# Optimization experiments

Hardware: AMD Instinct MI355X
Metric: run time of the kernel (lower is better)

Reference implementation:

```python
import jax, jax.numpy as jnp
import numpy as np

L = 2          # stacked LSTM layers
E = 4          # ensemble size
B, T, D = 256, 256, 512
H, CTX, HID, OUT = 512, 256, 256, 64


def setup_inputs() -> dict:
    key = jax.random.key(0)
    ks = jax.random.split(key, 16)
    w = lambda k, s, sc: (jax.random.normal(k, s, jnp.float32) * sc)
    r1 = lambda k, s: 1.0 + 0.05 * jax.random.normal(k, s, jnp.float32)
    lstm_b = jnp.zeros((L, E, 4 * H), jnp.float32).at[:, :, H:2 * H].set(1.0)  # unit forget bias
    return {
        'sequence_embeddings': jax.random.normal(ks[0], (B, T, D), jnp.float32),
        'context_embeddings': jax.random.normal(ks[1], (B, CTX), jnp.float32),
        'sequence_length': jax.random.randint(ks[2], (B,), 1, T + 1, jnp.int32),
        'lstm_W': w(ks[3], (L, D, 4 * H), 0.02),
        'lstm_U': w(ks[4], (L, H, 4 * H), 0.02),
        'lstm_b': lstm_b,
        'lstm_alpha': r1(ks[5], (L, E, D)),
        'lstm_gamma': r1(ks[6], (L, E, 4 * H)),
        'lstm_ralpha': r1(ks[7], (L, E, H)),
        'lstm_rgamma': r1(ks[8], (L, E, 4 * H)),
        'hid_W': w(ks[9], (H + CTX, HID), 0.05),
        'hid_b': jnp.zeros((E, HID), jnp.float32),
        'hid_alpha': r1(ks[10], (E, H + CTX)),
        'hid_gamma': r1(ks[11], (E, HID)),
        'out_W': w(ks[12], (HID, OUT), 0.05),
        'out_b': jnp.zeros((E, OUT), jnp.float32),
        'out_alpha': r1(ks[13], (E, HID)),
        'out_gamma': r1(ks[14], (E, OUT)),
    }


def reference(sequence_embeddings, context_embeddings, sequence_length,
              lstm_W, lstm_U, lstm_b, lstm_alpha, lstm_gamma, lstm_ralpha, lstm_rgamma,
              hid_W, hid_b, hid_alpha, hid_gamma,
              out_W, out_b, out_alpha, out_gamma):
    Bv, Tv, _ = sequence_embeddings.shape
    Hv = lstm_U.shape[1]
    per = Bv // E  # examples per ensemble member (consecutive blocks)
    exp = lambda p: jnp.repeat(p, per, axis=1)        # [L,E,d] -> [L,B,d]
    aF, gF = exp(lstm_alpha), exp(lstm_gamma)
    raF, rgF = exp(lstm_ralpha), exp(lstm_rgamma)
    bF = exp(lstm_b)

    dt = sequence_embeddings.dtype
    mask = (jnp.arange(Tv)[None, :] < sequence_length[:, None]).astype(dt)  # [B,T]
    xs = (jnp.swapaxes(sequence_embeddings, 0, 1), mask.T[..., None])       # [T,B,D], [T,B,1]

    def step(carry, xm):
        hs, cs = carry
        x, m = xm
        inp = x
        new_h, new_c = [], []
        for l in range(L):
            h, c = hs[l], cs[l]
            # rank-1 multiplicative perturbations fused with gate matmuls
            z = ((inp * aF[l]) @ lstm_W[l]) * gF[l] \
                + ((h * raF[l]) @ lstm_U[l]) * rgF[l] + bF[l]
            i, f, g, o = jnp.split(z, 4, axis=-1)
            c_n = jax.nn.sigmoid(f) * c + jax.nn.sigmoid(i) * jnp.tanh(g)
            h_n = jax.nn.sigmoid(o) * jnp.tanh(c_n)
            h_n = jnp.where(m > 0, h_n, h)  # masked steps carry state through
            c_n = jnp.where(m > 0, c_n, c)
            new_h.append(h_n)
            new_c.append(c_n)
            inp = h_n
        return (jnp.stack(new_h), jnp.stack(new_c)), None

    init = (jnp.zeros((L, Bv, Hv), dt), jnp.zeros((L, Bv, Hv), dt))
    (hs, _), _ = jax.lax.scan(step, init, xs)
    feat = jnp.concatenate([hs[-1], context_embeddings], axis=-1)

    def dense_r1(x, Wt, bt, al, ga, act=None):
        af = jnp.repeat(al, per, axis=0)
        gf = jnp.repeat(ga, per, axis=0)
        bf = jnp.repeat(bt, per, axis=0)
        y = ((x * af) @ Wt) * gf + bf
        return act(y) if act is not None else y

    relu6 = lambda v: jnp.clip(v, 0.0, 6.0)
    hidden = dense_r1(feat, hid_W, hid_b, hid_alpha, hid_gamma, relu6)
    return dense_r1(hidden, out_W, out_b, out_alpha, out_gamma)
```

## Files before the change

### kernel.cpp

```cpp
#include <hip/hip_runtime.h>
#include <cstdint>
#include <cstddef>


typedef __attribute__((ext_vector_type(8))) short  s16x8;
typedef __attribute__((ext_vector_type(8))) __bf16 bf16x8;
typedef __attribute__((ext_vector_type(4))) float  f32x4;
typedef unsigned long long ull;

__device__ __forceinline__ short f2bfs(float f) {
  union { float f; unsigned u; } v; v.f = f;
  unsigned r = v.u + 0x7FFFu + ((v.u >> 16) & 1u);
  return (short)(r >> 16);
}
__device__ __forceinline__ float bf2f(short s) {
  union { unsigned u; float f; } v; v.u = ((unsigned)(unsigned short)s) << 16;
  return v.f;
}
__device__ __forceinline__ void split2(float v, short& hi, short& lo) {
  hi = f2bfs(v);
  lo = f2bfs(v - bf2f(hi));
}
__device__ __forceinline__ float sigf(float x) { return 1.0f / (1.0f + __expf(-x)); }

__device__ __forceinline__ void unpack_pk(const uint4 r0, const uint4 r1,
                                          s16x8& hi, s16x8& lo) {
  uint4 hv, lv;
  hv.x = __builtin_amdgcn_perm(r0.y, r0.x, 0x05040100u);
  lv.x = __builtin_amdgcn_perm(r0.y, r0.x, 0x07060302u);
  hv.y = __builtin_amdgcn_perm(r0.w, r0.z, 0x05040100u);
  lv.y = __builtin_amdgcn_perm(r0.w, r0.z, 0x07060302u);
  hv.z = __builtin_amdgcn_perm(r1.y, r1.x, 0x05040100u);
  lv.z = __builtin_amdgcn_perm(r1.y, r1.x, 0x07060302u);
  hv.w = __builtin_amdgcn_perm(r1.w, r1.z, 0x05040100u);
  lv.w = __builtin_amdgcn_perm(r1.w, r1.z, 0x07060302u);
  hi = __builtin_bit_cast(s16x8, hv);
  lo = __builtin_bit_cast(s16x8, lv);
}

__device__ __forceinline__ void barrier_rb(unsigned* rbBase, int wgLocal,
                                           unsigned tstep) {
  __syncthreads();
  if (threadIdx.x < 64) {
    const int lane = threadIdx.x;
    int rel = 0;
    if (lane == 0) {
      const int c = wgLocal >> 3;
      unsigned a = __hip_atomic_fetch_add(rbBase + c * 16, 1u,
                                          __ATOMIC_RELAXED, __HIP_MEMORY_SCOPE_AGENT);
      if (a == 8u * tstep - 1u) {
        unsigned r = __hip_atomic_fetch_add(rbBase + 128, 1u,
                                            __ATOMIC_RELAXED, __HIP_MEMORY_SCOPE_AGENT);
        if (r == 8u * tstep - 1u) rel = 1;
      }
    }
    rel = __shfl(rel, 0);
    unsigned* flags = rbBase + 256;
    if (rel) {
      __hip_atomic_store(flags + lane * 16, tstep,
                         __ATOMIC_RELAXED, __HIP_MEMORY_SCOPE_AGENT);
    } else if (lane == 0) {
      int spins = 0;
      while (__hip_atomic_load(flags + wgLocal * 16, __ATOMIC_RELAXED,
                               __HIP_MEMORY_SCOPE_AGENT) < tstep) {
        __builtin_amdgcn_s_sleep(1);
        if (++spins > (1 << 22)) break;
      }
    }
    if (lane == 0)
      __builtin_amdgcn_fence(__ATOMIC_ACQUIRE, "agent");
  }
  __syncthreads();
}

#define REDOFF 131072

__global__ __launch_bounds__(512, 1) void lstm_persist(
    const unsigned* __restrict__ seqP,
    unsigned* __restrict__ h0P, unsigned* __restrict__ h1P,
    const short* __restrict__ Wf, const float* __restrict__ biasF,
    const int* __restrict__ slen, unsigned* __restrict__ bar)
{
  extern __shared__ __align__(16) char bsw[];
  const int wg = blockIdx.x;
  const int cls = wg & 7;
  const int layer = cls >> 2;
  const int rb = cls & 3;
  const int cb = wg >> 3;
  const int tid = threadIdx.x;
  const int wave = tid >> 6, lane = tid & 63;
  const int kh = wave >> 2, ws = wave & 3;
  const int wgLocal = (layer << 5) | cb;

  const short* Wfe = Wf + ((size_t)(layer * 4 + rb) * 2048 + cb * 64) * 1024;
  #pragma unroll
  for (int i = 0; i < 16; ++i) {
    int f = (i << 9) + tid;
    int col = f >> 7, fr = f & 127;
    s16x8 v = *reinterpret_cast<const s16x8*>(Wfe + (size_t)col * 1024 + (fr << 3));
    int byo = (fr << 10) + (((col << 4)) ^ ((fr & 7) << 4));
    *reinterpret_cast<s16x8*>(bsw + byo) = v;
  }
  __syncthreads();

  const int j = lane & 15;
  const int g = lane >> 4;
  const int koff = g << 3;
  const int rowg = rb * 64 + ws * 16 + j;
  const int rbase = rb * 64 + ws * 16 + (g << 2);
  const int u = cb * 16 + j;
  const float* bp = biasF + (size_t)(layer * 4 + rb) * 2048 + cb * 64 + j;
  const float bi = bp[0], bff = bp[16], bg = bp[32], bo = bp[48];
  int msl[4];
  #pragma unroll
  for (int r = 0; r < 4; ++r) msl[r] = slen[rbase + r];

  float creg[4] = {0.f, 0.f, 0.f, 0.f};
  float hreg[4] = {0.f, 0.f, 0.f, 0.f};
  const size_t BH = (size_t)256 * 512;
  unsigned* rbBase = bar + (rb << 11);
  const int fragbase = kh << 6;

  for (int t = 0; t <= 256; ++t) {
    const int s = t - layer;
    if (s >= 0 && s < 256) {
      const int cur = s & 1;
      const unsigned* hPrev = (layer ? h1P : h0P) + (size_t)cur * BH;
      unsigned* hOut = (layer ? h1P : h0P) + (size_t)(cur ^ 1) * BH;

      f32x4 acc[4] = {}, accL[4] = {};

      #define MMQ(FRAG, AHI, ALO)                                             \
        {                                                                     \
          const int fb_ = (FRAG) << 10;                                       \
          const int xm_ = ((FRAG) & 7) << 4;                                  \
          _Pragma("unroll")                                                   \
          for (int cf = 0; cf < 4; ++cf) {                                    \
            const int byo_ = fb_ + ((((cf << 8) | (j << 4))) ^ xm_);          \
            s16x8 b_ = *reinterpret_cast<const s16x8*>(bsw + byo_);           \
            acc[cf] = __builtin_amdgcn_mfma_f32_16x16x32_bf16(                \
                __builtin_bit_cast(bf16x8, AHI),                              \
                __builtin_bit_cast(bf16x8, b_), acc[cf], 0, 0, 0);            \
            accL[cf] = __builtin_amdgcn_mfma_f32_16x16x32_bf16(               \
                __builtin_bit_cast(bf16x8, ALO),                              \
                __builtin_bit_cast(bf16x8, b_), accL[cf], 0, 0, 0);           \
          }                                                                   \
        }

      const unsigned* ap;
      if (kh == 0 && layer == 0) {
        ap = seqP + (size_t)s * 131072 + (size_t)rowg * 512 + koff;
      } else if (kh == 0) {
        ap = h0P + (size_t)(cur ^ 1) * BH + (size_t)rowg * 512 + koff;
      } else {
        ap = hPrev + (size_t)rowg * 512 + koff;
      }
      #pragma unroll
      for (int blk = 0; blk < 2; ++blk) {
        uint4 R0[8], R1[8];
        #pragma unroll
        for (int q = 0; q < 8; ++q) {
          const unsigned* p = ap + (((blk << 3) | q) << 5);
          R0[q] = *reinterpret_cast<const uint4*>(p);
          R1[q] = *reinterpret_cast<const uint4*>(p + 4);
        }
        #pragma unroll
        for (int q = 0; q < 8; ++q) {
          s16x8 ahi, alo;
          unpack_pk(R0[q], R1[q], ahi, alo);
          MMQ((fragbase + ((((blk << 3) | q) << 2) | g)), ahi, alo)
        }
      }
      #undef MMQ

      if (kh == 1) {
        #pragma unroll
        for (int r = 0; r < 4; ++r) {
          const int lrow = ws * 16 + (g << 2) + r;
          f32x4 v = {acc[0][r] + accL[0][r], acc[1][r] + accL[1][r],
                     acc[2][r] + accL[2][r], acc[3][r] + accL[3][r]};
          *reinterpret_cast<f32x4*>(bsw + REDOFF + lrow * 256 + j * 16) = v;
        }
      }
      __syncthreads();
      if (kh == 0) {
        #pragma unroll
        for (int r = 0; r < 4; ++r) {
          const int lrow = ws * 16 + (g << 2) + r;
          f32x4 red = *reinterpret_cast<const f32x4*>(bsw + REDOFF + lrow * 256 + j * 16);
          const int row = rbase + r;
          float zi = acc[0][r] + accL[0][r] + red[0] + bi;
          float zf = acc[1][r] + accL[1][r] + red[1] + bff;
          float zg = acc[2][r] + accL[2][r] + red[2] + bg;
          float zo = acc[3][r] + accL[3][r] + red[3] + bo;
          float cn = sigf(zf) * creg[r] + sigf(zi) * tanhf(zg);
          float hn = sigf(zo) * tanhf(cn);
          if (s >= msl[r]) { cn = creg[r]; hn = hreg[r]; }
          creg[r] = cn; hreg[r] = hn;
          short hh, hl; split2(hn, hh, hl);
          unsigned pk = ((unsigned)(unsigned short)hl << 16)
                      | (unsigned)(unsigned short)hh;
          __hip_atomic_store(&hOut[(size_t)row * 512 + u], pk,
                             __ATOMIC_RELAXED, __HIP_MEMORY_SCOPE_AGENT);
        }
      }
    }
    if (t < 256) barrier_rb(rbBase, wgLocal, (unsigned)(t + 1));
  }
}

template<int EPI>
__global__ __launch_bounds__(256) void head_gemm(
    const unsigned* __restrict__ a0, int sA0,
    const unsigned* __restrict__ a1, int sA1, int kSplit,
    const short* __restrict__ Wh, const float* __restrict__ bias,
    int N, int K,
    unsigned* __restrict__ outP, float* __restrict__ outf)
{
  const int cb = blockIdx.x, rb = blockIdx.y;
  const int tid = threadIdx.x, wave = tid >> 6, lane = tid & 63;
  const int j = lane & 15;
  const int rowg = rb * 64 + wave * 16 + j;
  const int koff = (lane >> 4) << 3;
  const short* We = Wh + ((size_t)rb * N + cb * 64) * K;
  f32x4 acc[4] = {}, accL[4] = {};
  for (int ks = 0; ks < (K >> 5); ++ks) {
    const int kl = (ks << 5) + koff;
    const unsigned* ap = (kl < kSplit)
        ? (a0 + (size_t)rowg * sA0 + kl)
        : (a1 + (size_t)rowg * sA1 + (kl - kSplit));
    uint4 q0 = *reinterpret_cast<const uint4*>(ap);
    uint4 q1 = *reinterpret_cast<const uint4*>(ap + 4);
    s16x8 ahi, alo; unpack_pk(q0, q1, ahi, alo);
    #pragma unroll
    for (int cf = 0; cf < 4; ++cf) {
      const int ccol = (cf << 4) + j;
      s16x8 b = *reinterpret_cast<const s16x8*>(We + (size_t)ccol * K + kl);
      acc[cf] = __builtin_amdgcn_mfma_f32_16x16x32_bf16(
          __builtin_bit_cast(bf16x8, ahi), __builtin_bit_cast(bf16x8, b),
          acc[cf], 0, 0, 0);
      accL[cf] = __builtin_amdgcn_mfma_f32_16x16x32_bf16(
          __builtin_bit_cast(bf16x8, alo), __builtin_bit_cast(bf16x8, b),
          accL[cf], 0, 0, 0);
    }
  }
  const int rbase = rb * 64 + wave * 16 + ((lane >> 4) << 2);
  #pragma unroll
  for (int cf = 0; cf < 4; ++cf) {
    const int col = cb * 64 + cf * 16 + j;
    const float bb = bias[(size_t)rb * N + col];
    #pragma unroll
    for (int r = 0; r < 4; ++r) {
      float z = acc[cf][r] + accL[cf][r] + bb;
      if (EPI == 1) {
        z = fminf(fmaxf(z, 0.f), 6.f);
        short hh, hl; split2(z, hh, hl);
        outP[(size_t)(rbase + r) * N + col] =
            ((unsigned)(unsigned short)hl << 16) | (unsigned)(unsigned short)hh;
      } else {
        outf[(size_t)(rbase + r) * N + col] = z;
      }
    }
  }
}

__global__ __launch_bounds__(256) void fold_lstm(
    const float* __restrict__ W, const float* __restrict__ U,
    const float* __restrict__ al, const float* __restrict__ ral,
    const float* __restrict__ ga, const float* __restrict__ rga,
    short* __restrict__ Wf)
{
  __shared__ float T[64][65];
  const int tid = threadIdx.x;
  const int kb = blockIdx.x * 64;
  const int cb = blockIdx.y;
  const int le = blockIdx.z;
  const int l  = le >> 2;
  const int kl = tid >> 2;
  const int g  = tid & 3;
  const int k  = kb + kl;
  const bool isW = k < 512;
  const int kk = isW ? k : k - 512;
  const float* src = (isW ? W : U) + ((size_t)l * 512 + kk) * 2048;
  const float  a   = (isW ? al : ral)[(size_t)le * 512 + kk];
  const float* gam = (isW ? ga : rga) + (size_t)le * 2048;
  const int colBase = g * 512 + cb * 16;
  const float4* s4 = reinterpret_cast<const float4*>(src + colBase);
  const float4* g4 = reinterpret_cast<const float4*>(gam + colBase);
  #pragma unroll
  for (int q = 0; q < 4; ++q) {
    float4 v = s4[q], gv = g4[q];
    T[kl][g * 16 + q * 4 + 0] = v.x * a * gv.x;
    T[kl][g * 16 + q * 4 + 1] = v.y * a * gv.y;
    T[kl][g * 16 + q * 4 + 2] = v.z * a * gv.z;
    T[kl][g * 16 + q * 4 + 3] = v.w * a * gv.w;
  }
  __syncthreads();
  const int cl = tid >> 2, kq0 = (tid & 3) * 16;
  alignas(16) short tH[16];
  #pragma unroll
  for (int q = 0; q < 16; ++q) tH[q] = f2bfs(T[kq0 + q][cl]);
  size_t dst = ((size_t)le * 2048 + cb * 64 + cl) * 1024 + kb + kq0;
  *reinterpret_cast<s16x8*>(Wf + dst)     = *reinterpret_cast<s16x8*>(tH);
  *reinterpret_cast<s16x8*>(Wf + dst + 8) = *reinterpret_cast<s16x8*>(tH + 8);
}

__global__ __launch_bounds__(256) void fold_plain(
    const float* __restrict__ src, const float* __restrict__ al,
    const float* __restrict__ ga, short* __restrict__ dst, int N, int K)
{
  __shared__ float T[64][65];
  const int tid = threadIdx.x;
  const int kb = blockIdx.x * 64;
  const int nb = blockIdx.y;
  const int e  = blockIdx.z;
  const int kl = tid >> 2;
  const int c0 = (tid & 3) * 16;
  const int k  = kb + kl;
  const float a = al[(size_t)e * K + k];
  const int colBase = nb * 64 + c0;
  const float4* s4 = reinterpret_cast<const float4*>(src + (size_t)k * N + colBase);
  const float4* g4 = reinterpret_cast<const float4*>(ga + (size_t)e * N + colBase);
  #pragma unroll
  for (int q = 0; q < 4; ++q) {
    float4 v = s4[q], gv = g4[q];
    T[kl][c0 + q * 4 + 0] = v.x * a * gv.x;
    T[kl][c0 + q * 4 + 1] = v.y * a * gv.y;
    T[kl][c0 + q * 4 + 2] = v.z * a * gv.z;
    T[kl][c0 + q * 4 + 3] = v.w * a * gv.w;
  }
  __syncthreads();
  const int cl = tid >> 2, kq0 = (tid & 3) * 16;
  alignas(16) short tH[16];
  #pragma unroll
  for (int q = 0; q < 16; ++q) tH[q] = f2bfs(T[kq0 + q][cl]);
  size_t d = ((size_t)e * N + nb * 64 + cl) * K + kb + kq0;
  *reinterpret_cast<s16x8*>(dst + d)     = *reinterpret_cast<s16x8*>(tH);
  *reinterpret_cast<s16x8*>(dst + d + 8) = *reinterpret_cast<s16x8*>(tH + 8);
}

__global__ void fold_bias_lstm(const float* __restrict__ b, float* __restrict__ bf) {
  int idx = blockIdx.x * 256 + threadIdx.x;
  int cp = idx & 2047, le = idx >> 11;
  int ublk = cp >> 6, g = (cp >> 4) & 3, jj = cp & 15;
  bf[idx] = b[(size_t)le * 2048 + g * 512 + ublk * 16 + jj];
}

__global__ void cvt_pack(const float* __restrict__ s,
                         unsigned* __restrict__ d, int n) {
  int i = blockIdx.x * blockDim.x + threadIdx.x;
  if (i < n) {
    short h, l; split2(s[i], h, l);
    d[i] = ((unsigned)(unsigned short)l << 16) | (unsigned)(unsigned short)h;
  }
}

__global__ __launch_bounds__(128) void pack_seq(const float* __restrict__ s,
                                                unsigned* __restrict__ d) {
  const int t = blockIdx.x;
  const int row = blockIdx.y;
  const int d0 = threadIdx.x * 4;
  float4 v = *reinterpret_cast<const float4*>(
      s + ((size_t)row * 256 + t) * 512 + d0);
  uint4 o; short h, l;
  split2(v.x, h, l); o.x = ((unsigned)(unsigned short)l << 16) | (unsigned)(unsigned short)h;
  split2(v.y, h, l); o.y = ((unsigned)(unsigned short)l << 16) | (unsigned)(unsigned short)h;
  split2(v.z, h, l); o.z = ((unsigned)(unsigned short)l << 16) | (unsigned)(unsigned short)h;
  split2(v.w, h, l); o.w = ((unsigned)(unsigned short)l << 16) | (unsigned)(unsigned short)h;
  *reinterpret_cast<uint4*>(d + ((size_t)t * 256 + row) * 512 + d0) = o;
}

__global__ void zero_ws(float4* p, int n) {
  int i = blockIdx.x * blockDim.x + threadIdx.x;
  if (i < n) p[i] = make_float4(0.f, 0.f, 0.f, 0.f);
}

__global__ void init_bar(unsigned* bar) {
  int i = blockIdx.x * 256 + threadIdx.x;
  if (i < 8192) bar[i] = 0u;
}

constexpr size_t OFF_WF    = 0;
constexpr size_t OFF_WHID  = 33554432;
constexpr size_t OFF_WOUT  = OFF_WHID + 1572864;
constexpr size_t OFF_BIASF = OFF_WOUT + 131072;
constexpr size_t OFF_CTXP  = OFF_BIASF + 65536;
constexpr size_t OFF_H0P   = OFF_CTXP + 262144;
constexpr size_t OFF_H1P   = OFF_H0P + 1048576;
constexpr size_t OFF_HIDP  = OFF_H1P + 1048576;
constexpr size_t OFF_BAR   = OFF_HIDP + 262144;
constexpr size_t OFF_SEQP  = OFF_BAR + 32768;

extern "C" void kernel_launch(void* const* d_in, const int* in_sizes, int n_in,
                              void* d_out, int out_size, void* d_ws, size_t ws_size,
                              hipStream_t stream) {
  (void)in_sizes; (void)n_in; (void)out_size; (void)ws_size;
  const float* seq  = (const float*)d_in[0];
  const float* ctx  = (const float*)d_in[1];
  const int*   slen = (const int*)d_in[2];
  const float* lW   = (const float*)d_in[3];
  const float* lU   = (const float*)d_in[4];
  const float* lb   = (const float*)d_in[5];
  const float* lal  = (const float*)d_in[6];
  const float* lga  = (const float*)d_in[7];
  const float* lral = (const float*)d_in[8];
  const float* lrga = (const float*)d_in[9];
  const float* hW   = (const float*)d_in[10];
  const float* hb   = (const float*)d_in[11];
  const float* hal  = (const float*)d_in[12];
  const float* hga  = (const float*)d_in[13];
  const float* oW   = (const float*)d_in[14];
  const float* ob   = (const float*)d_in[15];
  const float* oal  = (const float*)d_in[16];
  const float* oga  = (const float*)d_in[17];

  char* ws = (char*)d_ws;
  short*    Wf    = (short*)(ws + OFF_WF);
  short*    Whid  = (short*)(ws + OFF_WHID);
  short*    Wout  = (short*)(ws + OFF_WOUT);
  float*    biasF = (float*)(ws + OFF_BIASF);
  unsigned* ctxP  = (unsigned*)(ws + OFF_CTXP);
  unsigned* h0P   = (unsigned*)(ws + OFF_H0P);
  unsigned* h1P   = (unsigned*)(ws + OFF_H1P);
  unsigned* hidP  = (unsigned*)(ws + OFF_HIDP);
  unsigned* bar   = (unsigned*)(ws + OFF_BAR);
  unsigned* seqP  = (unsigned*)(ws + OFF_SEQP);

  (void)hipFuncSetAttribute(reinterpret_cast<const void*>(lstm_persist),
                            hipFuncAttributeMaxDynamicSharedMemorySize, 147456);

  fold_lstm<<<dim3(16, 32, 8), 256, 0, stream>>>(lW, lU, lal, lral, lga, lrga, Wf);
  fold_plain<<<dim3(12, 4, 4), 256, 0, stream>>>(hW, hal, hga, Whid, 256, 768);
  fold_plain<<<dim3(4, 1, 4), 256, 0, stream>>>(oW, oal, oga, Wout, 64, 256);
  fold_bias_lstm<<<64, 256, 0, stream>>>(lb, biasF);
  cvt_pack<<<256, 256, 0, stream>>>(ctx, ctxP, 65536);
  pack_seq<<<dim3(256, 256), 128, 0, stream>>>(seq, seqP);
  zero_ws<<<512, 256, 0, stream>>>((float4*)(ws + OFF_H0P), 2097152 / 16);
  init_bar<<<32, 256, 0, stream>>>(bar);

  lstm_persist<<<256, 512, 147456, stream>>>(seqP, h0P, h1P, Wf, biasF, slen, bar);

  head_gemm<1><<<dim3(4, 4), 256, 0, stream>>>(
      h1P , 512,
      ctxP, 256, 512,
      Whid, hb, 256, 768, hidP, nullptr);
  head_gemm<2><<<dim3(1, 4), 256, 0, stream>>>(
      hidP, 256,
      hidP, 256, 256,
      Wout, ob, 64, 256,
      nullptr, (float*)d_out);
}
```

Baseline: 3.149 ms.

## Decouple LSTM layers with per-layer barriers and point-to-point progress counters

Replaces the joint barrier, which synchronized both layers together with a one-step skew, by per-(layer,row-block) group barriers. Cross-layer dependencies are now tracked through progress counters, so layer 1 can trail layer 0 by a variable amount. The layer-0 hidden state becomes a 4-slot ring buffer, which lets layer 0 run up to two steps ahead, and the two K-half loads are merged into one 16-deep load batch. It also swaps tanhf for an exp-based fast tanh. The aim is to cut barrier fan-in and remove lockstep stalls between layers, at the cost of extra workspace and more complex spin-wait logic.

```diff
diff --git a/kernel.cpp b/kernel.cpp
--- a/kernel.cpp
+++ b/kernel.cpp
@@ -22,6 +22,11 @@
   lo = f2bfs(v - bf2f(hi));
 }
 __device__ __forceinline__ float sigf(float x) { return 1.0f / (1.0f + __expf(-x)); }
+__device__ __forceinline__ float tanhf_fast(float x) {
+  float xc = fminf(fmaxf(x, -15.f), 15.f);
+  float e = __expf(2.f * xc);
+  return __fdividef(e - 1.f, e + 1.f);
+}
 
 __device__ __forceinline__ void unpack_pk(const uint4 r0, const uint4 r1,
                                           s16x8& hi, s16x8& lo) {
@@ -38,42 +43,55 @@
   lo = __builtin_bit_cast(s16x8, lv);
 }
 
-__device__ __forceinline__ void barrier_rb(unsigned* rbBase, int wgLocal,
-                                           unsigned tstep) {
+#define HIP_RLX __ATOMIC_RELAXED
+#define HIP_AGT __HIP_MEMORY_SCOPE_AGENT
+
+__device__ __forceinline__ void step_sync(unsigned* grpBase, unsigned* Pme,
+                                          unsigned* Pother, int cb,
+                                          unsigned tstep, int pneed) {
   __syncthreads();
   if (threadIdx.x < 64) {
     const int lane = threadIdx.x;
     int rel = 0;
     if (lane == 0) {
-      const int c = wgLocal >> 3;
-      unsigned a = __hip_atomic_fetch_add(rbBase + c * 16, 1u,
-                                          __ATOMIC_RELAXED, __HIP_MEMORY_SCOPE_AGENT);
+      unsigned a = __hip_atomic_fetch_add(grpBase + ((cb >> 3) << 4), 1u,
+                                          HIP_RLX, HIP_AGT);
       if (a == 8u * tstep - 1u) {
-        unsigned r = __hip_atomic_fetch_add(rbBase + 128, 1u,
-                                            __ATOMIC_RELAXED, __HIP_MEMORY_SCOPE_AGENT);
-        if (r == 8u * tstep - 1u) rel = 1;
+        unsigned r = __hip_atomic_fetch_add(grpBase + 64, 1u, HIP_RLX, HIP_AGT);
+        if (r == 4u * tstep - 1u) rel = 1;
       }
     }
     rel = __shfl(rel, 0);
-    unsigned* flags = rbBase + 256;
+    unsigned* flags = grpBase + 128;
     if (rel) {
-      __hip_atomic_store(flags + lane * 16, tstep,
-                         __ATOMIC_RELAXED, __HIP_MEMORY_SCOPE_AGENT);
-    } else if (lane == 0) {
-      int spins = 0;
-      while (__hip_atomic_load(flags + wgLocal * 16, __ATOMIC_RELAXED,
-                               __HIP_MEMORY_SCOPE_AGENT) < tstep) {
-        __builtin_amdgcn_s_sleep(1);
-        if (++spins > (1 << 22)) break;
-      }
-    }
-    if (lane == 0)
+      if (lane < 32)
+        __hip_atomic_store(flags + lane * 16, tstep, HIP_RLX, HIP_AGT);
+      if (lane == 0)
+        __hip_atomic_store(Pme, tstep, HIP_RLX, HIP_AGT);
+    }
+    if (lane == 0) {
+      if (!rel) {
+        int spins = 0;
+        while (__hip_atomic_load(flags + cb * 16, HIP_RLX, HIP_AGT) < tstep) {
+          __builtin_amdgcn_s_sleep(1);
+          if (++spins > (1 << 24)) break;
+        }
+      }
+      if (pneed > 0) {
+        int spins = 0;
+        while ((int)__hip_atomic_load(Pother, HIP_RLX, HIP_AGT) < pneed) {
+          __builtin_amdgcn_s_sleep(1);
+          if (++spins > (1 << 24)) break;
+        }
+      }
       __builtin_amdgcn_fence(__ATOMIC_ACQUIRE, "agent");
+    }
   }
   __syncthreads();
 }
 
 #define REDOFF 131072
+#define BHU 131072
 
 __global__ __launch_bounds__(512, 1) void lstm_persist(
     const unsigned* __restrict__ seqP,
@@ -90,7 +108,6 @@
   const int tid = threadIdx.x;
   const int wave = tid >> 6, lane = tid & 63;
   const int kh = wave >> 2, ws = wave & 3;
-  const int wgLocal = (layer << 5) | cb;
 
   const short* Wfe = Wf + ((size_t)(layer * 4 + rb) * 2048 + cb * 64) * 1024;
   #pragma unroll
@@ -117,95 +134,99 @@
 
   float creg[4] = {0.f, 0.f, 0.f, 0.f};
   float hreg[4] = {0.f, 0.f, 0.f, 0.f};
-  const size_t BH = (size_t)256 * 512;
-  unsigned* rbBase = bar + (rb << 11);
+  unsigned* grpBase = bar + (cls << 10);
+  unsigned* Pme     = bar + 8192 + (cls << 4);
+  unsigned* Pother  = bar + 8192 + ((cls ^ 4) << 4);
   const int fragbase = kh << 6;
 
-  for (int t = 0; t <= 256; ++t) {
-    const int s = t - layer;
-    if (s >= 0 && s < 256) {
-      const int cur = s & 1;
-      const unsigned* hPrev = (layer ? h1P : h0P) + (size_t)cur * BH;
-      unsigned* hOut = (layer ? h1P : h0P) + (size_t)(cur ^ 1) * BH;
-
-      f32x4 acc[4] = {}, accL[4] = {};
-
-      #define MMQ(FRAG, AHI, ALO)                                             \
-        {                                                                     \
-          const int fb_ = (FRAG) << 10;                                       \
-          const int xm_ = ((FRAG) & 7) << 4;                                  \
-          _Pragma("unroll")                                                   \
-          for (int cf = 0; cf < 4; ++cf) {                                    \
-            const int byo_ = fb_ + ((((cf << 8) | (j << 4))) ^ xm_);          \
-            s16x8 b_ = *reinterpret_cast<const s16x8*>(bsw + byo_);           \
-            acc[cf] = __builtin_amdgcn_mfma_f32_16x16x32_bf16(                \
-                __builtin_bit_cast(bf16x8, AHI),                              \
-                __builtin_bit_cast(bf16x8, b_), acc[cf], 0, 0, 0);            \
-            accL[cf] = __builtin_amdgcn_mfma_f32_16x16x32_bf16(               \
-                __builtin_bit_cast(bf16x8, ALO),                              \
-                __builtin_bit_cast(bf16x8, b_), accL[cf], 0, 0, 0);           \
-          }                                                                   \
-        }
-
-      const unsigned* ap;
-      if (kh == 0 && layer == 0) {
-        ap = seqP + (size_t)s * 131072 + (size_t)rowg * 512 + koff;
-      } else if (kh == 0) {
-        ap = h0P + (size_t)(cur ^ 1) * BH + (size_t)rowg * 512 + koff;
-      } else {
-        ap = hPrev + (size_t)rowg * 512 + koff;
-      }
+  if (tid == 0) {
+    if (layer == 1) {
+      int spins = 0;
+      while (__hip_atomic_load(Pother, HIP_RLX, HIP_AGT) < 1u) {
+        __builtin_amdgcn_s_sleep(1);
+        if (++spins > (1 << 24)) break;
+      }
+    }
+    __builtin_amdgcn_fence(__ATOMIC_ACQUIRE, "agent");
+  }
+  __syncthreads();
+
+  for (int t = 0; t < 256; ++t) {
+    const unsigned* ap;
+    if (kh == 0) {
+      ap = (layer == 0)
+         ? seqP + (size_t)t * 131072 + (size_t)rowg * 512 + koff
+         : h0P + (size_t)((t + 1) & 3) * BHU + (size_t)rowg * 512 + koff;
+    } else {
+      ap = (layer == 0)
+         ? h0P + (size_t)(t & 3) * BHU + (size_t)rowg * 512 + koff
+         : h1P + (size_t)(t & 1) * BHU + (size_t)rowg * 512 + koff;
+    }
+
+    uint4 R0[16], R1[16];
+    #pragma unroll
+    for (int q = 0; q < 16; ++q) {
+      R0[q] = *reinterpret_cast<const uint4*>(ap + (q << 5));
+      R1[q] = *reinterpret_cast<const uint4*>(ap + (q << 5) + 4);
+    }
+
+    f32x4 acc[4] = {}, accL[4] = {};
+    #pragma unroll
+    for (int q = 0; q < 16; ++q) {
+      s16x8 ahi, alo;
+      unpack_pk(R0[q], R1[q], ahi, alo);
+      const int frag = fragbase + ((q << 2) | g);
+      const int fb_ = frag << 10;
+      const int xm_ = (frag & 7) << 4;
       #pragma unroll
-      for (int blk = 0; blk < 2; ++blk) {
-        uint4 R0[8], R1[8];
-        #pragma unroll
-        for (int q = 0; q < 8; ++q) {
-          const unsigned* p = ap + (((blk << 3) | q) << 5);
-          R0[q] = *reinterpret_cast<const uint4*>(p);
-          R1[q] = *reinterpret_cast<const uint4*>(p + 4);
-        }
-        #pragma unroll
-        for (int q = 0; q < 8; ++q) {
-          s16x8 ahi, alo;
-          unpack_pk(R0[q], R1[q], ahi, alo);
-          MMQ((fragbase + ((((blk << 3) | q) << 2) | g)), ahi, alo)
-        }
-      }
-      #undef MMQ
-
-      if (kh == 1) {
-        #pragma unroll
-        for (int r = 0; r < 4; ++r) {
-          const int lrow = ws * 16 + (g << 2) + r;
-          f32x4 v = {acc[0][r] + accL[0][r], acc[1][r] + accL[1][r],
-                     acc[2][r] + accL[2][r], acc[3][r] + accL[3][r]};
-          *reinterpret_cast<f32x4*>(bsw + REDOFF + lrow * 256 + j * 16) = v;
-        }
-      }
-      __syncthreads();
-      if (kh == 0) {
-        #pragma unroll
-        for (int r = 0; r < 4; ++r) {
-          const int lrow = ws * 16 + (g << 2) + r;
-          f32x4 red = *reinterpret_cast<const f32x4*>(bsw + REDOFF + lrow * 256 + j * 16);
-          const int row = rbase + r;
-          float zi = acc[0][r] + accL[0][r] + red[0] + bi;
-          float zf = acc[1][r] + accL[1][r] + red[1] + bff;
-          float zg = acc[2][r] + accL[2][r] + red[2] + bg;
-          float zo = acc[3][r] + accL[3][r] + red[3] + bo;
-          float cn = sigf(zf) * creg[r] + sigf(zi) * tanhf(zg);
-          float hn = sigf(zo) * tanhf(cn);
-          if (s >= msl[r]) { cn = creg[r]; hn = hreg[r]; }
-          creg[r] = cn; hreg[r] = hn;
-          short hh, hl; split2(hn, hh, hl);
-          unsigned pk = ((unsigned)(unsigned short)hl << 16)
-                      | (unsigned)(unsigned short)hh;
-          __hip_atomic_store(&hOut[(size_t)row * 512 + u], pk,
-                             __ATOMIC_RELAXED, __HIP_MEMORY_SCOPE_AGENT);
-        }
-      }
-    }
-    if (t < 256) barrier_rb(rbBase, wgLocal, (unsigned)(t + 1));
+      for (int cf = 0; cf < 4; ++cf) {
+        const int byo_ = fb_ + ((((cf << 8) | (j << 4))) ^ xm_);
+        s16x8 b_ = *reinterpret_cast<const s16x8*>(bsw + byo_);
+        acc[cf] = __builtin_amdgcn_mfma_f32_16x16x32_bf16(
+            __builtin_bit_cast(bf16x8, ahi), __builtin_bit_cast(bf16x8, b_),
+            acc[cf], 0, 0, 0);
+        accL[cf] = __builtin_amdgcn_mfma_f32_16x16x32_bf16(
+            __builtin_bit_cast(bf16x8, alo), __builtin_bit_cast(bf16x8, b_),
+            accL[cf], 0, 0, 0);
+      }
+    }
+
+    if (kh == 1) {
+      #pragma unroll
+      for (int r = 0; r < 4; ++r) {
+        const int lrow = ws * 16 + (g << 2) + r;
+        f32x4 v = {acc[0][r] + accL[0][r], acc[1][r] + accL[1][r],
+                   acc[2][r] + accL[2][r], acc[3][r] + accL[3][r]};
+        *reinterpret_cast<f32x4*>(bsw + REDOFF + lrow * 256 + j * 16) = v;
+      }
+    }
+    __syncthreads();
+    if (kh == 0) {
+      unsigned* hOut = (layer == 0)
+          ? h0P + (size_t)((t + 1) & 3) * BHU
+          : h1P + (size_t)((t & 1) ^ 1) * BHU;
+      #pragma unroll
+      for (int r = 0; r < 4; ++r) {
+        const int lrow = ws * 16 + (g << 2) + r;
+        f32x4 red = *reinterpret_cast<const f32x4*>(bsw + REDOFF + lrow * 256 + j * 16);
+        const int row = rbase + r;
+        float zi = acc[0][r] + accL[0][r] + red[0] + bi;
+        float zf = acc[1][r] + accL[1][r] + red[1] + bff;
+        float zg = acc[2][r] + accL[2][r] + red[2] + bg;
+        float zo = acc[3][r] + accL[3][r] + red[3] + bo;
+        float cn = sigf(zf) * creg[r] + sigf(zi) * tanhf_fast(zg);
+        float hn = sigf(zo) * tanhf_fast(cn);
+        if (t >= msl[r]) { cn = creg[r]; hn = hreg[r]; }
+        creg[r] = cn; hreg[r] = hn;
+        short hh, hl; split2(hn, hh, hl);
+        unsigned pk = ((unsigned)(unsigned short)hl << 16)
+                    | (unsigned)(unsigned short)hh;
+        __hip_atomic_store(&hOut[(size_t)row * 512 + u], pk, HIP_RLX, HIP_AGT);
+      }
+    }
+
+    int pneed = (t < 255) ? (layer == 0 ? t - 2 : t + 2) : 0;
+    step_sync(grpBase, Pme, Pother, cb, (unsigned)(t + 1), pneed);
   }
 }
 
@@ -377,7 +398,7 @@
 
 __global__ void init_bar(unsigned* bar) {
   int i = blockIdx.x * 256 + threadIdx.x;
-  if (i < 8192) bar[i] = 0u;
+  if (i < 16384) bar[i] = 0u;
 }
 
 constexpr size_t OFF_WF    = 0;
@@ -386,10 +407,10 @@
 constexpr size_t OFF_BIASF = OFF_WOUT + 131072;
 constexpr size_t OFF_CTXP  = OFF_BIASF + 65536;
 constexpr size_t OFF_H0P   = OFF_CTXP + 262144;
-constexpr size_t OFF_H1P   = OFF_H0P + 1048576;
+constexpr size_t OFF_H1P   = OFF_H0P + 2097152;
 constexpr size_t OFF_HIDP  = OFF_H1P + 1048576;
 constexpr size_t OFF_BAR   = OFF_HIDP + 262144;
-constexpr size_t OFF_SEQP  = OFF_BAR + 32768;
+constexpr size_t OFF_SEQP  = OFF_BAR + 65536;
 
 extern "C" void kernel_launch(void* const* d_in, const int* in_sizes, int n_in,
                               void* d_out, int out_size, void* d_ws, size_t ws_size,
@@ -435,8 +456,8 @@
   fold_bias_lstm<<<64, 256, 0, stream>>>(lb, biasF);
   cvt_pack<<<256, 256, 0, stream>>>(ctx, ctxP, 65536);
   pack_seq<<<dim3(256, 256), 128, 0, stream>>>(seq, seqP);
-  zero_ws<<<512, 256, 0, stream>>>((float4*)(ws + OFF_H0P), 2097152 / 16);
-  init_bar<<<32, 256, 0, stream>>>(bar);
+  zero_ws<<<768, 256, 0, stream>>>((float4*)(ws + OFF_H0P), 3145728 / 16);
+  init_bar<<<64, 256, 0, stream>>>(bar);
 
   lstm_persist<<<256, 512, 147456, stream>>>(seqP, h0P, h1P, Wf, biasF, slen, bar);
 
```

New measurement: 3.080 ms. 2.2% less time.
